# Kernel optimization log

Hardware: AMD Instinct MI355X
Metric: run time of the kernel (lower is better)

## Reference

```python
import jax, jax.numpy as jnp
import numpy as np

N = 100000   # nodes
E = 1600000  # edges
IN = 128
H = 128
OUT = 64
G = 512      # graphs in batch


def setup_inputs() -> dict:
    key = jax.random.key(0)
    ks = jax.random.split(key, 9)
    x = jax.random.normal(ks[0], (N, IN), jnp.float32)
    edge_index = jax.random.randint(ks[1], (2, E), 0, N, dtype=jnp.int64)
    batch = jnp.sort(jax.random.randint(ks[2], (N,), 0, G, dtype=jnp.int64))
    # Glorot-ish init for weights, zeros for biases (as in GCNConv / nn.Linear defaults)
    W1 = jax.random.normal(ks[3], (IN, H), jnp.float32) * (1.0 / np.sqrt(IN))
    b1 = jnp.zeros((H,), jnp.float32)
    W2 = jax.random.normal(ks[4], (H, H), jnp.float32) * (1.0 / np.sqrt(H))
    b2 = jnp.zeros((H,), jnp.float32)
    Wl = jax.random.normal(ks[5], (H, OUT), jnp.float32) * (1.0 / np.sqrt(H))
    bl = jnp.zeros((OUT,), jnp.float32)
    return dict(x=x, edge_index=edge_index, batch=batch,
                W1=W1, b1=b1, W2=W2, b2=b2, Wl=Wl, bl=bl)


def reference(x, edge_index, batch, W1, b1, W2, b2, Wl, bl):
    n = x.shape[0]
    loop = jnp.arange(n, dtype=edge_index.dtype)
    # GCNConv default: add self-loops, symmetric normalization D^-1/2 A D^-1/2
    src = jnp.concatenate([edge_index[0], loop])  # message sources
    dst = jnp.concatenate([edge_index[1], loop])  # aggregation targets
    deg = jax.ops.segment_sum(jnp.ones(src.shape[0], jnp.float32), dst, num_segments=n)
    dinv = jnp.where(deg > 0, jax.lax.rsqrt(deg), 0.0)
    norm = dinv[src] * dinv[dst]  # [E+N]

    def gcn_conv(h, W, b):
        h = h @ W                              # [N, H] linear transform first
        msg = h[src] * norm[:, None]           # gather + scale: [E+N, H]
        return jax.ops.segment_sum(msg, dst, num_segments=n) + b

    h = jax.nn.relu(gcn_conv(x, W1, b1))
    # dropout: eval mode (training=False) -> identity
    h = jax.nn.relu(gcn_conv(h, W2, b2))
    pooled = jax.ops.segment_sum(h, batch, num_segments=G)  # global_add_pool: [G, H]
    return pooled @ Wl + bl
```

## Files before the change

kernel.cpp:

```cpp
#include <hip/hip_runtime.h>
#include <hip/hip_bf16.h>

typedef unsigned short u16;
typedef unsigned int   u32;
typedef unsigned long long u64;
typedef long long      i64;
typedef __attribute__((ext_vector_type(8))) short short8;
typedef __attribute__((ext_vector_type(4))) float f32x4;

#define HD 128
#define OUTD 64
#define BSH 8
#define NBKT_MAX 512
#define PCHUNK 2048
#define EPB 4096
#define GCUR_STRIDE 16

__device__ __forceinline__ float bf2f(u16 u){ union{u32 i; float f;} x; x.i=((u32)u)<<16; return x.f; }
__device__ __forceinline__ u16 f2bf(float f){ __hip_bfloat16 h=__float2bfloat16(f); return *reinterpret_cast<u16*>(&h); }
__device__ __forceinline__ float blo(u32 v){ union{u32 i; float f;} x; x.i=v<<16; return x.f; }
__device__ __forceinline__ float bhi(u32 v){ union{u32 i; float f;} x; x.i=v&0xffff0000u; return x.f; }

__device__ __forceinline__ short8 load8(const float* p){
  f32x4 lo = *reinterpret_cast<const f32x4*>(p);
  f32x4 hi = *reinterpret_cast<const f32x4*>(p + 4);
  short8 r;
  #pragma unroll
  for (int j=0;j<4;j++){ r[j]=(short)f2bf(lo[j]); r[4+j]=(short)f2bf(hi[j]); }
  return r;
}
__device__ __forceinline__ short8 load8(const u16* p){
  return *reinterpret_cast<const short8*>(p);
}

__device__ __forceinline__ int idx_at(const void* p, int i, int is32){
  return is32 ? ((const int*)p)[i] : (int)((const i64*)p)[i];
}

__global__ void k_zero_out(float* __restrict__ out, int n){
  int i = blockIdx.x*256 + threadIdx.x;
  if (i < n) out[i] = 0.f;
}

__global__ __launch_bounds__(256) void k_pack_w(
    const float* __restrict__ W1, u16* __restrict__ Wp1,
    const float* __restrict__ W2, u16* __restrict__ Wp2)
{
  const float* W  = blockIdx.x ? W2 : W1;
  u16*         Wp = blockIdx.x ? Wp2 : Wp1;
  for (int u = threadIdx.x; u < 2048; u += 256){
    int lane = u & 63, tc = u >> 6;
    int t = tc >> 2, c = tc & 3;
    int n = lane & 15, quad = lane >> 4;
    #pragma unroll
    for (int j=0;j<8;j++)
      Wp[(size_t)u*8 + j] = f2bf(W[(c*32 + quad*8 + j)*HD + t*16 + n]);
  }
}

__global__ __launch_bounds__(256) void k_init(
    const u32* __restrict__ ei, const u32* __restrict__ bw,
    int* __restrict__ flags, int* __restrict__ bcntp, float* __restrict__ pooled,
    int npairs_e, int npairs_b, int nbc, int npool)
{
  int t = threadIdx.x;
  if (blockIdx.x == 0){
    if (t < 16) flags[t] = 0;
    __syncthreads();
    for (int i=t; i<npairs_e; i+=256) if (ei[2*i+1] != 0) atomicOr(&flags[0], 1);
    for (int i=t; i<npairs_b; i+=256) if (bw[2*i+1] != 0) atomicOr(&flags[1], 1);
  } else {
    int i = (blockIdx.x-1)*256 + t;
    if (i < nbc)   bcntp[i] = 0;
    if (i < npool) pooled[i] = 0.f;
  }
}

__global__ __launch_bounds__(256) void k_bucket_sorted(
    const void* __restrict__ batch, const void* __restrict__ ei,
    int* __restrict__ flags, int* __restrict__ bcntp, int n, int E, int NBc)
{
  __shared__ int hist[NBKT_MAX];
  int tid = threadIdx.x;
  if (blockIdx.x < NBc){
    int i = blockIdx.x*256 + tid;
    if (i < n-1){
      int is32 = flags[1];
      if (idx_at(batch, i, is32) > idx_at(batch, i+1, is32)) atomicOr(&flags[2], 1);
    }
    return;
  }
  hist[tid]=0; hist[tid+256]=0;
  __syncthreads();
  int base = (blockIdx.x - NBc)*EPB;
  int is32 = flags[0];
  #pragma unroll
  for (int k=0;k<EPB/256;k++){
    int e = base + k*256 + tid;
    if (e < E){
      int d = idx_at(ei, E + e, is32);
      atomicAdd(&hist[d>>BSH], 1);
    }
  }
  __syncthreads();
  int a0=hist[2*tid], a1=hist[2*tid+1];
  if (a0) atomicAdd(&bcntp[(2*tid)*GCUR_STRIDE],   a0);
  if (a1) atomicAdd(&bcntp[(2*tid+1)*GCUR_STRIDE], a1);
}

__global__ __launch_bounds__(256) void k_bucket_scan(
    const int* __restrict__ bcntp, int* __restrict__ gcur, int* __restrict__ bbase,
    int* __restrict__ row_ptr, int N, int E)
{
  __shared__ int scant[256];
  int t = threadIdx.x;
  int a0 = bcntp[(2*t)*GCUR_STRIDE], a1 = bcntp[(2*t+1)*GCUR_STRIDE];
  scant[t] = a0 + a1; __syncthreads();
  for (int o=1;o<256;o<<=1){ int x=(t>=o)?scant[t-o]:0; __syncthreads(); scant[t]+=x; __syncthreads(); }
  int pre = (t>0)?scant[t-1]:0;
  gcur[(2*t)*GCUR_STRIDE]   = pre;      bbase[2*t]   = pre;
  gcur[(2*t+1)*GCUR_STRIDE] = pre + a0; bbase[2*t+1] = pre + a0;
  if (t == 255){ bbase[512] = pre + a0 + a1; row_ptr[N] = E; }
}

__global__ __launch_bounds__(256) void k_part1(
    const void* __restrict__ ei, const int* __restrict__ flags,
    int* __restrict__ gcur, u32* __restrict__ pairs, int E)
{
  __shared__ int hist[NBKT_MAX];
  __shared__ int soff[NBKT_MAX];
  __shared__ int gb[NBKT_MAX];
  __shared__ int scant[256];
  __shared__ u32 stage[PCHUNK];
  __shared__ u16 sbkt[PCHUNK];

  int tid = threadIdx.x;
  hist[tid]=0; hist[tid+256]=0;
  __syncthreads();

  int base = blockIdx.x*PCHUNK;
  int is32 = flags[0];
  int d[PCHUNK/256], s[PCHUNK/256];
  #pragma unroll
  for (int k=0;k<PCHUNK/256;k++){
    int e = base + k*256 + tid;
    if (e < E){
      d[k]=idx_at(ei,E+e,is32); s[k]=idx_at(ei,e,is32);
      atomicAdd(&hist[d[k]>>BSH],1);
    } else d[k]=-1;
  }
  __syncthreads();

  int a0=hist[2*tid], a1=hist[2*tid+1];
  scant[tid]=a0+a1; __syncthreads();
  for (int o=1;o<256;o<<=1){ int x2=(tid>=o)?scant[tid-o]:0; __syncthreads(); scant[tid]+=x2; __syncthreads(); }
  int pre = (tid>0)?scant[tid-1]:0;
  soff[2*tid]=pre; soff[2*tid+1]=pre+a0;
  if (a0) gb[2*tid]   = atomicAdd(&gcur[(2*tid)*GCUR_STRIDE],   a0); else gb[2*tid]=0;
  if (a1) gb[2*tid+1] = atomicAdd(&gcur[(2*tid+1)*GCUR_STRIDE], a1); else gb[2*tid+1]=0;
  hist[2*tid]=0; hist[2*tid+1]=0;
  __syncthreads();

  #pragma unroll
  for (int k=0;k<PCHUNK/256;k++){
    if (d[k]>=0){
      int b = d[k]>>BSH;
      int loc = soff[b] + atomicAdd(&hist[b],1);
      stage[loc] = (u32)s[k] | ((u32)(d[k] & ((1<<BSH)-1)) << 24);
      sbkt[loc] = (u16)b;
    }
  }
  __syncthreads();

  int cnt_edges = E - base; if (cnt_edges > PCHUNK) cnt_edges = PCHUNK;
  for (int i=tid; i<cnt_edges; i+=256){
    int b = sbkt[i];
    pairs[(size_t)gb[b] + (i - soff[b])] = stage[i];
  }
}

__global__ __launch_bounds__(256) void k_part2ex(
    const u32* __restrict__ pairs, const int* __restrict__ bbase,
    int* __restrict__ row_ptr, float* __restrict__ dinv,
    int* __restrict__ colv, int N)
{
  __shared__ int lcnt[1<<BSH];
  __shared__ int sscan[256];
  __shared__ int lcur[1<<BSH];
  int b = blockIdx.x, t = threadIdx.x;
  int n0 = b<<BSH;
  int nn = N - n0; if (nn > 256) nn = 256;
  int lo = bbase[b], hi = bbase[b+1];
  lcnt[t] = 0; lcur[t] = lo;
  __syncthreads();
  for (int i = lo + t; i < hi; i += 256)
    atomicAdd(&lcnt[pairs[i] >> 24], 1);
  __syncthreads();
  int c = lcnt[t];
  sscan[t] = c; __syncthreads();
  for (int o=1;o<256;o<<=1){ int x=(t>=o)?sscan[t-o]:0; __syncthreads(); sscan[t]+=x; __syncthreads(); }
  int pre = (t>0)?sscan[t-1]:0;
  if (t < nn){
    row_ptr[n0+t] = lo + pre;
    dinv[n0+t]    = rsqrtf((float)(c+1));
    lcur[t]       = lo + pre;
  }
  __syncthreads();
  for (int i = lo + t; i < hi; i += 256){
    u32 p = pairs[i];
    int pos = atomicAdd(&lcur[p>>24], 1);
    if (pos >= lo && pos < hi) colv[pos] = (int)(p & 0xFFFFFFu);
  }
}

template <typename TIN>
__global__ __launch_bounds__(256) void k_gemm_scale(
    const TIN* __restrict__ X, const u16* __restrict__ Wp,
    const float* __restrict__ dinv, u16* __restrict__ Gout, int nrows)
{
  int lane = threadIdx.x & 63;
  int wv   = threadIdx.x >> 6;
  int n    = lane & 15, quad = lane >> 4;

  const short8* wp = reinterpret_cast<const short8*>(Wp);
  short8 bf[8][4];
  #pragma unroll
  for (int t=0;t<8;t++)
    #pragma unroll
    for (int c=0;c<4;c++)
      bf[t][c] = wp[(t*4+c)*64 + lane];

  int ntiles = (nrows+15)>>4;
  int stride = gridDim.x*4;
  for (int tile = blockIdx.x*4 + wv; tile < ntiles; tile += stride){
    int ra = tile*16 + n;
    if (ra >= nrows) ra = nrows-1;
    const TIN* xp = X + (size_t)ra*HD + quad*8;
    short8 a[4];
    #pragma unroll
    for (int c=0;c<4;c++) a[c] = load8(xp + c*32);

    f32x4 acc[8];
    #pragma unroll
    for (int t=0;t<8;t++) acc[t] = (f32x4){0.f,0.f,0.f,0.f};
    #pragma unroll
    for (int c=0;c<4;c++)
      #pragma unroll
      for (int t=0;t<8;t++)
        acc[t] = __builtin_amdgcn_mfma_f32_16x16x32_bf16(a[c], bf[t][c], acc[t], 0,0,0);

    float dv[4]; int rw[4];
    #pragma unroll
    for (int r=0;r<4;r++){
      int row = tile*16 + quad*4 + r;
      rw[r]=row; dv[r]=(row<nrows)?dinv[row]:0.f;
    }
    #pragma unroll
    for (int t=0;t<8;t++)
      #pragma unroll
      for (int r=0;r<4;r++){
        int row = rw[r];
        if (row < nrows)
          Gout[(size_t)row*HD + t*16 + n] = f2bf(dv[r]*acc[t][r]);
      }
  }
}

__global__ __launch_bounds__(256) void k_aggregate(
    const u16* __restrict__ g, const int* __restrict__ row_ptr,
    const int* __restrict__ colv, const float* __restrict__ dinv,
    const float* __restrict__ bias, u16* __restrict__ h, int n)
{
  int node = blockIdx.x*4 + (threadIdx.x>>6);
  if (node >= n) return;
  int lane = threadIdx.x & 63;
  int off = lane*2;

  u32 u = *reinterpret_cast<const u32*>(g + (size_t)node*HD + off);
  float ax = blo(u), ay = bhi(u);

  int s = row_ptr[node], e = row_ptr[node+1];
  int i = s;
  for (; i+16<=e; i+=16){
    u32 v[16];
    #pragma unroll
    for (int j=0;j<16;j++)
      v[j] = *reinterpret_cast<const u32*>(g+(size_t)colv[i+j]*HD+off);
    #pragma unroll
    for (int j=0;j<16;j++){ ax += blo(v[j]); ay += bhi(v[j]); }
  }
  if (i+8<=e){
    u32 v[8];
    #pragma unroll
    for (int j=0;j<8;j++)
      v[j] = *reinterpret_cast<const u32*>(g+(size_t)colv[i+j]*HD+off);
    #pragma unroll
    for (int j=0;j<8;j++){ ax += blo(v[j]); ay += bhi(v[j]); }
    i += 8;
  }
  if (i+4<=e){
    u32 v[4];
    #pragma unroll
    for (int j=0;j<4;j++)
      v[j] = *reinterpret_cast<const u32*>(g+(size_t)colv[i+j]*HD+off);
    #pragma unroll
    for (int j=0;j<4;j++){ ax += blo(v[j]); ay += bhi(v[j]); }
    i += 4;
  }
  for (; i<e; i++){
    u32 v=*reinterpret_cast<const u32*>(g+(size_t)colv[i]*HD+off);
    ax += blo(v); ay += bhi(v);
  }

  float dv = dinv[node];
  float rx = fmaxf(fmaf(dv, ax, bias[off]),   0.f);
  float ry = fmaxf(fmaf(dv, ay, bias[off+1]), 0.f);
  *reinterpret_cast<u32*>(h + (size_t)node*HD + off) = (u32)f2bf(rx) | ((u32)f2bf(ry)<<16);
}

__device__ __forceinline__ int lowerb(const void* a, int is32, int n, int key){
  int lo=0, hi=n;
  while (lo<hi){
    int mid=(lo+hi)>>1;
    if (idx_at(a, mid, is32) < key) lo=mid+1; else hi=mid;
  }
  return lo;
}

__global__ __launch_bounds__(256) void k_pool_final_sorted(
    const u16* __restrict__ h, const void* __restrict__ batch,
    const int* __restrict__ flags, const float* __restrict__ Wl,
    const float* __restrict__ bl, float* __restrict__ out, int n)
{
  if (flags[2]) return;
  __shared__ float sd[4][128];
  __shared__ float ps[128];
  __shared__ float racc[4][64];
  int gid = blockIdx.x, t = threadIdx.x;
  int w = t >> 6, lane = t & 63;
  int off = lane*2;
  int is32 = flags[1];
  int lo = lowerb(batch, is32, n, gid), hi = lowerb(batch, is32, n, gid+1);

  float ax = 0.f, ay = 0.f;
  int i = lo + w;
  for (; i + 12 < hi; i += 16){
    u32 v0 = *reinterpret_cast<const u32*>(h + (size_t)(i   )*HD + off);
    u32 v1 = *reinterpret_cast<const u32*>(h + (size_t)(i+ 4)*HD + off);
    u32 v2 = *reinterpret_cast<const u32*>(h + (size_t)(i+ 8)*HD + off);
    u32 v3 = *reinterpret_cast<const u32*>(h + (size_t)(i+12)*HD + off);
    ax += blo(v0)+blo(v1)+blo(v2)+blo(v3);
    ay += bhi(v0)+bhi(v1)+bhi(v2)+bhi(v3);
  }
  for (; i < hi; i += 4){
    u32 v = *reinterpret_cast<const u32*>(h + (size_t)i*HD + off);
    ax += blo(v); ay += bhi(v);
  }
  sd[w][off] = ax; sd[w][off+1] = ay;
  __syncthreads();
  if (t < 128) ps[t] = sd[0][t] + sd[1][t] + sd[2][t] + sd[3][t];
  __syncthreads();

  int o = t & 63, seg = t >> 6;
  float acc = 0.f;
  #pragma unroll
  for (int kk=0; kk<32; kk++){
    int k = seg*32 + kk;
    acc = fmaf(ps[k], Wl[k*OUTD + o], acc);
  }
  racc[seg][o] = acc;
  __syncthreads();
  if (t < 64)
    out[(size_t)gid*OUTD + t] = bl[t] + racc[0][t] + racc[1][t] + racc[2][t] + racc[3][t];
}

__global__ __launch_bounds__(256) void k_pool_atomic(
    const u16* __restrict__ h, const void* __restrict__ batch,
    const int* __restrict__ flags, float* __restrict__ pooled, int n)
{
  if (!flags[2]) return;
  int lane = threadIdx.x & 63;
  int off = lane*2;
  int is32 = flags[1];
  for (int node = blockIdx.x*4 + (threadIdx.x>>6); node < n; node += gridDim.x*4){
    int g = idx_at(batch, node, is32);
    u32 v = *reinterpret_cast<const u32*>(h + (size_t)node*HD + off);
    atomicAdd(&pooled[(size_t)g*HD + off],     blo(v));
    atomicAdd(&pooled[(size_t)g*HD + off + 1], bhi(v));
  }
}

__global__ void k_final(const float* __restrict__ pooled, const float* __restrict__ Wl,
                        const float* __restrict__ bl, const int* __restrict__ flags,
                        float* __restrict__ out){
  if (!flags[2]) return;
  int gid = blockIdx.x, t = threadIdx.x;
  float acc = bl[t];
  const float* p = pooled + gid*HD;
  #pragma unroll 8
  for (int k=0;k<HD;k++) acc = fmaf(p[k], Wl[k*OUTD + t], acc);
  out[gid*OUTD + t] = acc;
}

extern "C" void kernel_launch(void* const* d_in, const int* in_sizes, int n_in,
                              void* d_out, int out_size, void* d_ws, size_t ws_size,
                              hipStream_t stream)
{
  const float* x   = (const float*)d_in[0];
  const void*  ei  = d_in[1];
  const void*  bat = d_in[2];
  const float* W1  = (const float*)d_in[3];
  const float* b1  = (const float*)d_in[4];
  const float* W2  = (const float*)d_in[5];
  const float* b2  = (const float*)d_in[6];
  const float* Wl  = (const float*)d_in[7];
  const float* bl  = (const float*)d_in[8];
  float* out = (float*)d_out;

  int N = in_sizes[0] / HD;
  int E = in_sizes[1] / 2;
  int G = out_size / OUTD;
  int nbins = (N + (1<<BSH) - 1) >> BSH;

  char* w = (char*)d_ws;
  size_t o = 0;
  auto alloc = [&](size_t b){ void* p = w + o; o += (b + 255) & ~(size_t)255; return p; };
  int*   row_ptr = (int*)  alloc((size_t)(N+1)*4);
  int*   colv    = (int*)  alloc((size_t)E*4);
  u32*   pairs   = (u32*)  alloc((size_t)E*4);
  int*   gcur    = (int*)  alloc((size_t)NBKT_MAX*GCUR_STRIDE*4);
  int*   bcntp   = (int*)  alloc((size_t)NBKT_MAX*GCUR_STRIDE*4);
  int*   bbase   = (int*)  alloc((size_t)(NBKT_MAX+1)*4);
  float* dinv    = (float*)alloc((size_t)N*4);
  u16*   gbuf    = (u16*)  alloc((size_t)N*HD*2);
  u16*   hbuf    = (u16*)  alloc((size_t)N*HD*2);
  float* pooled  = (float*)alloc((size_t)G*HD*4);
  u16*   wp1     = (u16*)  alloc((size_t)HD*HD*2);
  u16*   wp2     = (u16*)  alloc((size_t)HD*HD*2);
  int*   flags   = (int*)  alloc(256);
  (void)n_in;

  if (o > ws_size || nbins > NBKT_MAX){
    k_zero_out<<<(out_size+255)/256, 256, 0, stream>>>(out, out_size);
    return;
  }

  int npairs_e = 4096; if (npairs_e > E) npairs_e = E;
  int npairs_b = 4096; if (npairs_b > N/2) npairs_b = N/2;
  int npool = G*HD;
  int nbc = NBKT_MAX*GCUR_STRIDE;
  int nzb = (npool+255)/256; { int bz = (nbc+255)/256; if (bz > nzb) nzb = bz; }

  k_pack_w<<<2, 256, 0, stream>>>(W1, wp1, W2, wp2);
  k_init<<<1+nzb, 256, 0, stream>>>((const u32*)ei, (const u32*)bat, flags, bcntp, pooled,
                                    npairs_e, npairs_b, nbc, npool);
  int NBc = (N+255)/256, NPB = (E+EPB-1)/EPB;
  k_bucket_sorted<<<NBc+NPB, 256, 0, stream>>>(bat, ei, flags, bcntp, N, E, NBc);
  k_bucket_scan<<<1, 256, 0, stream>>>(bcntp, gcur, bbase, row_ptr, N, E);
  int npart = (E + PCHUNK - 1) / PCHUNK;
  k_part1<<<npart, 256, 0, stream>>>(ei, flags, gcur, pairs, E);
  k_part2ex<<<nbins, 256, 0, stream>>>(pairs, bbase, row_ptr, dinv, colv, N);
  k_gemm_scale<float><<<512, 256, 0, stream>>>(x, wp1, dinv, gbuf, N);
  k_aggregate <<<(N+3)/4, 256, 0, stream>>>(gbuf, row_ptr, colv, dinv, b1, hbuf, N);
  k_gemm_scale<u16><<<512, 256, 0, stream>>>(hbuf, wp2, dinv, gbuf, N);
  k_aggregate <<<(N+3)/4, 256, 0, stream>>>(gbuf, row_ptr, colv, dinv, b2, hbuf, N);
  k_pool_final_sorted<<<G, 256, 0, stream>>>(hbuf, bat, flags, Wl, bl, out, N);
  k_pool_atomic<<<1024, 256, 0, stream>>>(hbuf, bat, flags, pooled, N);
  k_final      <<<G, OUTD, 0, stream>>>(pooled, Wl, bl, flags, out);
}
```

Measured before the change: 369.6 us.

## Merge weight packing into init, fuse pooling kernels, split aggregation launches

Folds the weight-packing kernel into the init kernel and merges the sorted-pool and atomic-pool kernels into one launch, with block index choosing the path. This cuts the number of kernel launches. Each aggregation is also split into four launches over contiguous node ranges, which adds launches and looks like an experiment in cache locality or scheduling. That split may add launch overhead and tail effects.

```diff
diff --git a/kernel.cpp b/kernel.cpp
--- a/kernel.cpp
+++ b/kernel.cpp
@@ -42,35 +42,32 @@
   if (i < n) out[i] = 0.f;
 }
 
-__global__ __launch_bounds__(256) void k_pack_w(
+__global__ __launch_bounds__(256) void k_init(
     const float* __restrict__ W1, u16* __restrict__ Wp1,
-    const float* __restrict__ W2, u16* __restrict__ Wp2)
-{
-  const float* W  = blockIdx.x ? W2 : W1;
-  u16*         Wp = blockIdx.x ? Wp2 : Wp1;
-  for (int u = threadIdx.x; u < 2048; u += 256){
-    int lane = u & 63, tc = u >> 6;
-    int t = tc >> 2, c = tc & 3;
-    int n = lane & 15, quad = lane >> 4;
-    #pragma unroll
-    for (int j=0;j<8;j++)
-      Wp[(size_t)u*8 + j] = f2bf(W[(c*32 + quad*8 + j)*HD + t*16 + n]);
-  }
-}
-
-__global__ __launch_bounds__(256) void k_init(
+    const float* __restrict__ W2, u16* __restrict__ Wp2,
     const u32* __restrict__ ei, const u32* __restrict__ bw,
     int* __restrict__ flags, int* __restrict__ bcntp, float* __restrict__ pooled,
     int npairs_e, int npairs_b, int nbc, int npool)
 {
   int t = threadIdx.x;
-  if (blockIdx.x == 0){
+  if (blockIdx.x < 2){
+    const float* W  = blockIdx.x ? W2 : W1;
+    u16*         Wp = blockIdx.x ? Wp2 : Wp1;
+    for (int u = t; u < 2048; u += 256){
+      int lane = u & 63, tc = u >> 6;
+      int tt = tc >> 2, c = tc & 3;
+      int n = lane & 15, quad = lane >> 4;
+      #pragma unroll
+      for (int j=0;j<8;j++)
+        Wp[(size_t)u*8 + j] = f2bf(W[(c*32 + quad*8 + j)*HD + tt*16 + n]);
+    }
+  } else if (blockIdx.x == 2){
     if (t < 16) flags[t] = 0;
     __syncthreads();
     for (int i=t; i<npairs_e; i+=256) if (ei[2*i+1] != 0) atomicOr(&flags[0], 1);
     for (int i=t; i<npairs_b; i+=256) if (bw[2*i+1] != 0) atomicOr(&flags[1], 1);
   } else {
-    int i = (blockIdx.x-1)*256 + t;
+    int i = (blockIdx.x-3)*256 + t;
     if (i < nbc)   bcntp[i] = 0;
     if (i < npool) pooled[i] = 0.f;
   }
@@ -269,10 +266,10 @@
 __global__ __launch_bounds__(256) void k_aggregate(
     const u16* __restrict__ g, const int* __restrict__ row_ptr,
     const int* __restrict__ colv, const float* __restrict__ dinv,
-    const float* __restrict__ bias, u16* __restrict__ h, int n)
-{
-  int node = blockIdx.x*4 + (threadIdx.x>>6);
-  if (node >= n) return;
+    const float* __restrict__ bias, u16* __restrict__ h, int rn0, int rn1)
+{
+  int node = rn0 + blockIdx.x*4 + (threadIdx.x>>6);
+  if (node >= rn1) return;
   int lane = threadIdx.x & 63;
   int off = lane*2;
 
@@ -327,19 +324,35 @@
   return lo;
 }
 
-__global__ __launch_bounds__(256) void k_pool_final_sorted(
+__global__ __launch_bounds__(256) void k_pool_final(
     const u16* __restrict__ h, const void* __restrict__ batch,
     const int* __restrict__ flags, const float* __restrict__ Wl,
-    const float* __restrict__ bl, float* __restrict__ out, int n)
-{
-  if (flags[2]) return;
+    const float* __restrict__ bl, float* __restrict__ out,
+    float* __restrict__ pooled, int n, int G)
+{
   __shared__ float sd[4][128];
   __shared__ float ps[128];
   __shared__ float racc[4][64];
-  int gid = blockIdx.x, t = threadIdx.x;
+  int t = threadIdx.x;
+  int is32 = flags[1];
+
+  if (blockIdx.x >= G){
+    if (!flags[2]) return;
+    int lane = t & 63;
+    int off = lane*2;
+    for (int node = (blockIdx.x-G)*4 + (t>>6); node < n; node += 1024*4){
+      int g = idx_at(batch, node, is32);
+      u32 v = *reinterpret_cast<const u32*>(h + (size_t)node*HD + off);
+      atomicAdd(&pooled[(size_t)g*HD + off],     blo(v));
+      atomicAdd(&pooled[(size_t)g*HD + off + 1], bhi(v));
+    }
+    return;
+  }
+  if (flags[2]) return;
+
+  int gid = blockIdx.x;
   int w = t >> 6, lane = t & 63;
   int off = lane*2;
-  int is32 = flags[1];
   int lo = lowerb(batch, is32, n, gid), hi = lowerb(batch, is32, n, gid+1);
 
   float ax = 0.f, ay = 0.f;
@@ -372,22 +385,6 @@
   __syncthreads();
   if (t < 64)
     out[(size_t)gid*OUTD + t] = bl[t] + racc[0][t] + racc[1][t] + racc[2][t] + racc[3][t];
-}
-
-__global__ __launch_bounds__(256) void k_pool_atomic(
-    const u16* __restrict__ h, const void* __restrict__ batch,
-    const int* __restrict__ flags, float* __restrict__ pooled, int n)
-{
-  if (!flags[2]) return;
-  int lane = threadIdx.x & 63;
-  int off = lane*2;
-  int is32 = flags[1];
-  for (int node = blockIdx.x*4 + (threadIdx.x>>6); node < n; node += gridDim.x*4){
-    int g = idx_at(batch, node, is32);
-    u32 v = *reinterpret_cast<const u32*>(h + (size_t)node*HD + off);
-    atomicAdd(&pooled[(size_t)g*HD + off],     blo(v));
-    atomicAdd(&pooled[(size_t)g*HD + off + 1], bhi(v));
-  }
 }
 
 __global__ void k_final(const float* __restrict__ pooled, const float* __restrict__ Wl,
@@ -451,8 +448,8 @@
   int nbc = NBKT_MAX*GCUR_STRIDE;
   int nzb = (npool+255)/256; { int bz = (nbc+255)/256; if (bz > nzb) nzb = bz; }
 
-  k_pack_w<<<2, 256, 0, stream>>>(W1, wp1, W2, wp2);
-  k_init<<<1+nzb, 256, 0, stream>>>((const u32*)ei, (const u32*)bat, flags, bcntp, pooled,
+  k_init<<<3+nzb, 256, 0, stream>>>(W1, wp1, W2, wp2,
+                                    (const u32*)ei, (const u32*)bat, flags, bcntp, pooled,
                                     npairs_e, npairs_b, nbc, npool);
   int NBc = (N+255)/256, NPB = (E+EPB-1)/EPB;
   k_bucket_sorted<<<NBc+NPB, 256, 0, stream>>>(bat, ei, flags, bcntp, N, E, NBc);
@@ -460,11 +457,17 @@
   int npart = (E + PCHUNK - 1) / PCHUNK;
   k_part1<<<npart, 256, 0, stream>>>(ei, flags, gcur, pairs, E);
   k_part2ex<<<nbins, 256, 0, stream>>>(pairs, bbase, row_ptr, dinv, colv, N);
+  int qn = (N+3)/4;
   k_gemm_scale<float><<<512, 256, 0, stream>>>(x, wp1, dinv, gbuf, N);
-  k_aggregate <<<(N+3)/4, 256, 0, stream>>>(gbuf, row_ptr, colv, dinv, b1, hbuf, N);
+  for (int k=0;k<4;k++){
+    int a=k*qn, b=(k+1)*qn; if (b>N) b=N;
+    if (b>a) k_aggregate<<<(b-a+3)/4, 256, 0, stream>>>(gbuf, row_ptr, colv, dinv, b1, hbuf, a, b);
+  }
   k_gemm_scale<u16><<<512, 256, 0, stream>>>(hbuf, wp2, dinv, gbuf, N);
-  k_aggregate <<<(N+3)/4, 256, 0, stream>>>(gbuf, row_ptr, colv, dinv, b2, hbuf, N);
-  k_pool_final_sorted<<<G, 256, 0, stream>>>(hbuf, bat, flags, Wl, bl, out, N);
-  k_pool_atomic<<<1024, 256, 0, stream>>>(hbuf, bat, flags, pooled, N);
-  k_final      <<<G, OUTD, 0, stream>>>(pooled, Wl, bl, flags, out);
-}
+  for (int k=0;k<4;k++){
+    int a=k*qn, b=(k+1)*qn; if (b>N) b=N;
+    if (b>a) k_aggregate<<<(b-a+3)/4, 256, 0, stream>>>(gbuf, row_ptr, colv, dinv, b2, hbuf, a, b);
+  }
+  k_pool_final<<<G+1024, 256, 0, stream>>>(hbuf, bat, flags, Wl, bl, out, pooled, N, G);
+  k_final     <<<G, OUTD, 0, stream>>>(pooled, Wl, bl, flags, out);
+}
```

New measurement: 393.8 us. 6.5% more time.
